# Performance work log

Measured on AMD Instinct MI355X. Metric: run time of the kernel, lower is better.

Reference implementation:

```python
import jax, jax.numpy as jnp
import numpy as np

EPS = 1e-6
NUM_HEADS = 4
GSIZE = (2, 2, 2)


def _ln_channels_first(x, w, b):
    # LayerNorm over channel dim (axis=1) of [B,C,D,H,W]
    u = x.mean(1, keepdims=True)
    s = ((x - u) ** 2).mean(1, keepdims=True)
    xn = (x - u) / jnp.sqrt(s + EPS)
    return w[None, :, None, None, None] * xn + b[None, :, None, None, None]


def setup_inputs() -> dict:
    key = jax.random.key(0)
    ks = jax.random.split(key, 7)
    B, C = 2, 256
    x2 = jax.random.normal(ks[0], (B, C, 32, 32, 32), jnp.float32)
    x1_low = jax.random.normal(ks[1], (B, C, 16, 16, 16), jnp.float32)
    sc = 1.0 / np.sqrt(C).astype(np.float32)
    q_w = jax.random.normal(ks[2], (C, C), jnp.float32) * sc
    k_w = jax.random.normal(ks[3], (C, C), jnp.float32) * sc
    v_w = jax.random.normal(ks[4], (C, C), jnp.float32) * sc
    dw_w = jax.random.normal(ks[5], (C, 1, 3, 3, 3), jnp.float32) * (1.0 / np.sqrt(27.0).astype(np.float32))
    proj_w = jax.random.normal(ks[6], (C, C), jnp.float32) * sc
    nq_w = jnp.ones((C,), jnp.float32)
    nq_b = jnp.zeros((C,), jnp.float32)
    nkv_w = jnp.ones((C,), jnp.float32)
    nkv_b = jnp.zeros((C,), jnp.float32)
    return {"x2": x2, "x1_low": x1_low, "q_w": q_w, "k_w": k_w, "v_w": v_w,
            "dw_w": dw_w, "proj_w": proj_w, "nq_w": nq_w, "nq_b": nq_b,
            "nkv_w": nkv_w, "nkv_b": nkv_b}


def reference(x2, x1_low, q_w, k_w, v_w, dw_w, proj_w, nq_w, nq_b, nkv_w, nkv_b):
    B, C, D, H, W = x2.shape
    h = NUM_HEADS
    d = C // h
    gD, gH, gW = GSIZE
    _, _, Dl, Hl, Wl = x1_low.shape

    # adaptive_avg_pool3d to (gD,gH,gW): dims divisible -> block means
    tokens = x1_low.reshape(B, C, gD, Dl // gD, gH, Hl // gH, gW, Wl // gW).mean((3, 5, 7))
    # depthwise 3x3x3 conv, padding 1
    dw = jax.lax.conv_general_dilated(
        tokens, dw_w, window_strides=(1, 1, 1), padding='SAME',
        dimension_numbers=('NCDHW', 'OIDHW', 'NCDHW'), feature_group_count=C)
    tokens = tokens + dw

    N = D * H * W
    g = gD * gH * gW

    qx = _ln_channels_first(x2, nq_w, nq_b).reshape(B, C, N)
    q = jnp.einsum('oc,bcn->bon', q_w, qx).reshape(B, h, d, N).transpose(0, 1, 3, 2)  # [B,h,N,d]

    tk = _ln_channels_first(tokens, nkv_w, nkv_b).reshape(B, C, g)
    k = jnp.einsum('oc,bcg->bog', k_w, tk).reshape(B, h, d, g)  # [B,h,d,g]
    v = jnp.einsum('oc,bcg->bog', v_w, tokens.reshape(B, C, g)).reshape(B, h, d, g).transpose(0, 1, 3, 2)  # [B,h,g,d]

    attn = jax.nn.softmax(jnp.einsum('bhnd,bhdg->bhng', q, k) / jnp.sqrt(jnp.float32(d)), axis=-1)
    out = jnp.einsum('bhng,bhgd->bhnd', attn, v)  # [B,h,N,d]
    out = out.transpose(0, 1, 3, 2).reshape(B, C, N)
    return jnp.einsum('oc,bcn->bon', proj_w, out).reshape(B, C, D, H, W)
```

## Files before the change

### kernel.cpp

```cpp
#include <hip/hip_runtime.h>
#include <math.h>

#define EPS 1e-6f

typedef __attribute__((ext_vector_type(8))) short bhalf8;
typedef __attribute__((ext_vector_type(4))) float floatx4;

__device__ __forceinline__ unsigned short f2bf(float f) {
    union { float f; unsigned u; } v; v.f = f;
    unsigned r = (v.u + 0x7fffu + ((v.u >> 16) & 1u)) >> 16;
    return (unsigned short)r;
}
__device__ __forceinline__ float bflo(unsigned u) {
    union { unsigned x; float f; } v; v.x = u << 16; return v.f;
}
__device__ __forceinline__ float bfhi(unsigned u) {
    union { unsigned x; float f; } v; v.x = u & 0xffff0000u; return v.f;
}

__global__ void pre1(const float* __restrict__ q_w,
                     const float* __restrict__ proj_w,
                     const float* __restrict__ nq_w,
                     const float* __restrict__ nq_b,
                     float* __restrict__ W1, float* __restrict__ W2,
                     unsigned short* __restrict__ W1b,
                     unsigned short* __restrict__ W2b,
                     float* __restrict__ A, float* __restrict__ Bc,
                     const float* __restrict__ x1, float* __restrict__ tokens) {
    if (blockIdx.x < 256) {
        int o = blockIdx.x;
        int c = threadIdx.x;
        float qv = q_w[o * 256 + c];
        float pv = proj_w[o * 256 + c];
        float w1 = qv * nq_w[c];
        W1[c * 256 + o] = w1;
        W2[c * 256 + o] = pv;
        int kc = c >> 5, kk = c & 31;
        W1b[kc * 8192 + o * 32 + kk] = f2bf(w1);
        W2b[kc * 8192 + o * 32 + kk] = f2bf(pv);
        float bcv = qv * nq_b[c];
        __shared__ float sA[4], sB[4];
        float a = w1, b = bcv;
        for (int off = 32; off > 0; off >>= 1) {
            a += __shfl_down(a, off);
            b += __shfl_down(b, off);
        }
        int wave = threadIdx.x >> 6, lane = threadIdx.x & 63;
        if (lane == 0) { sA[wave] = a; sB[wave] = b; }
        __syncthreads();
        if (threadIdx.x == 0) {
            A[o]  = sA[0] + sA[1] + sA[2] + sA[3];
            Bc[o] = sB[0] + sB[1] + sB[2] + sB[3];
        }
    } else {
        int bc = blockIdx.x - 256;
        const float* base = x1 + (size_t)bc * 4096;
        int wave = threadIdx.x >> 6;
        int lane = threadIdx.x & 63;
        int doff = lane >> 3, hoff = lane & 7;
        for (int t = wave * 2; t < wave * 2 + 2; ++t) {
            int gd = t >> 2, gh = (t >> 1) & 1, gw = t & 1;
            const float* p = base + (gd * 8 + doff) * 256 + (gh * 8 + hoff) * 16 + gw * 8;
            float4 v0 = *(const float4*)p;
            float4 v1 = *(const float4*)(p + 4);
            float s = v0.x + v0.y + v0.z + v0.w + v1.x + v1.y + v1.z + v1.w;
            for (int off = 32; off > 0; off >>= 1) s += __shfl_down(s, off);
            if (lane == 0) tokens[bc * 8 + t] = s * (1.0f / 512.0f);
        }
    }
}

__global__ void tokens_prep(const float* __restrict__ tokens,
                            const float* __restrict__ dw_w,
                            const float* __restrict__ nkv_w,
                            const float* __restrict__ nkv_b,
                            float* __restrict__ t2g, float* __restrict__ tng) {
    int b = blockIdx.x;
    int c = threadIdx.x;
    __shared__ float t2[256][8];
    __shared__ float u8[8], r8[8];
    float t[8];
    #pragma unroll
    for (int g = 0; g < 8; ++g) t[g] = tokens[(b * 256 + c) * 8 + g];
    float w[27];
    #pragma unroll
    for (int i = 0; i < 27; ++i) w[i] = dw_w[c * 27 + i];
    #pragma unroll
    for (int z = 0; z < 2; ++z)
    #pragma unroll
    for (int y = 0; y < 2; ++y)
    #pragma unroll
    for (int x = 0; x < 2; ++x) {
        float s = 0.f;
        #pragma unroll
        for (int i = 0; i < 3; ++i) {
            int nz = z + i - 1; if (nz < 0 || nz > 1) continue;
            #pragma unroll
            for (int j = 0; j < 3; ++j) {
                int ny = y + j - 1; if (ny < 0 || ny > 1) continue;
                #pragma unroll
                for (int l = 0; l < 3; ++l) {
                    int nx = x + l - 1; if (nx < 0 || nx > 1) continue;
                    s += w[(i * 3 + j) * 3 + l] * t[nz * 4 + ny * 2 + nx];
                }
            }
        }
        int g = z * 4 + y * 2 + x;
        t2[c][g] = t[g] + s;
    }
    __syncthreads();
    if (c < 8) {
        float su = 0.f, sq = 0.f;
        for (int cc = 0; cc < 256; ++cc) { float v = t2[cc][c]; su += v; sq += v * v; }
        float u = su * (1.f / 256.f);
        float var = sq * (1.f / 256.f) - u * u;
        u8[c] = u;
        r8[c] = rsqrtf(var + EPS);
    }
    __syncthreads();
    float nw = nkv_w[c], nb = nkv_b[c];
    #pragma unroll
    for (int g = 0; g < 8; ++g) {
        float tv = t2[c][g];
        t2g[(b * 256 + c) * 8 + g] = tv;
        tng[(b * 256 + c) * 8 + g] = nw * (tv - u8[g]) * r8[g] + nb;
    }
}

__global__ void tokens_proj(const float* __restrict__ k_w,
                            const float* __restrict__ v_w,
                            const float* __restrict__ t2g,
                            const float* __restrict__ tng,
                            float* __restrict__ kk, float* __restrict__ vv,
                            unsigned short* __restrict__ kkb) {
    int b = blockIdx.x >> 6;
    int og = blockIdx.x & 63;
    int w = threadIdx.x >> 6;
    int lane = threadIdx.x & 63;
    int o = og * 4 + w;
    float acck[8] = {0,0,0,0,0,0,0,0}, accv[8] = {0,0,0,0,0,0,0,0};
    #pragma unroll
    for (int i = 0; i < 4; ++i) {
        int c = lane + 64 * i;
        float kw = k_w[o * 256 + c];
        float vw = v_w[o * 256 + c];
        const float* tb = t2g + (size_t)(b * 256 + c) * 8;
        const float* nb = tng + (size_t)(b * 256 + c) * 8;
        float4 ta0 = *(const float4*)tb;
        float4 ta1 = *(const float4*)(tb + 4);
        float4 tn0 = *(const float4*)nb;
        float4 tn1 = *(const float4*)(nb + 4);
        acck[0] += kw * tn0.x; acck[1] += kw * tn0.y; acck[2] += kw * tn0.z; acck[3] += kw * tn0.w;
        acck[4] += kw * tn1.x; acck[5] += kw * tn1.y; acck[6] += kw * tn1.z; acck[7] += kw * tn1.w;
        accv[0] += vw * ta0.x; accv[1] += vw * ta0.y; accv[2] += vw * ta0.z; accv[3] += vw * ta0.w;
        accv[4] += vw * ta1.x; accv[5] += vw * ta1.y; accv[6] += vw * ta1.z; accv[7] += vw * ta1.w;
    }
    #pragma unroll
    for (int g = 0; g < 8; ++g)
        for (int off = 32; off > 0; off >>= 1) {
            acck[g] += __shfl_down(acck[g], off);
            accv[g] += __shfl_down(accv[g], off);
        }
    if (lane == 0) {
        #pragma unroll
        for (int g = 0; g < 8; ++g) {
            int ki = b * 2048 + o * 8 + g;
            int vi = b * 2048 + (o >> 6) * 512 + g * 64 + (o & 63);
            kk[ki] = acck[g];
            kkb[ki] = f2bf(acck[g]);
            vv[vi] = accv[g];
        }
    }
}

__global__ void ln_stats(const float* __restrict__ x2,
                         float* __restrict__ u, float* __restrict__ r) {
    int t = blockIdx.x * blockDim.x + threadIdx.x;
    int n = t << 2;
    int b = n >> 15;
    int pos = n & 32767;
    const float* p = x2 + (size_t)b * 8388608 + pos;
    float su0 = 0, su1 = 0, su2 = 0, su3 = 0;
    float sq0 = 0, sq1 = 0, sq2 = 0, sq3 = 0;
    for (int c = 0; c < 256; ++c) {
        float4 v = *(const float4*)(p + (size_t)c * 32768);
        su0 += v.x; sq0 += v.x * v.x;
        su1 += v.y; sq1 += v.y * v.y;
        su2 += v.z; sq2 += v.z * v.z;
        su3 += v.w; sq3 += v.w * v.w;
    }
    const float inv = 1.f / 256.f;
    float4 um, rm;
    um.x = su0 * inv; um.y = su1 * inv; um.z = su2 * inv; um.w = su3 * inv;
    rm.x = rsqrtf(sq0 * inv - um.x * um.x + EPS);
    rm.y = rsqrtf(sq1 * inv - um.y * um.y + EPS);
    rm.z = rsqrtf(sq2 * inv - um.z * um.z + EPS);
    rm.w = rsqrtf(sq3 * inv - um.w * um.w + EPS);
    *(float4*)(u + n) = um;
    *(float4*)(r + n) = rm;
}

__global__ __launch_bounds__(256, 3)
void fused_mfma(const float* __restrict__ x2,
                const unsigned short* __restrict__ W1b,
                const unsigned short* __restrict__ W2b,
                const float* __restrict__ Ag, const float* __restrict__ Bg,
                const unsigned short* __restrict__ kkb,
                const float* __restrict__ vvf,
                float* __restrict__ out) {
    __shared__ __align__(16) unsigned short XQ[16384];
    __shared__ __align__(16) float KVP[3072];
    __shared__ float As[256], Bs[256], us[64], rs[64];

    const int tid = threadIdx.x;
    const int w = tid >> 6;
    const int lane = tid & 63;
    const int n0g = blockIdx.x * 64;
    const int b = n0g >> 15;

    uint4  kreg  = ((const uint4*)(kkb + b * 2048))[tid];
    float4 vreg0 = ((const float4*)(vvf + b * 2048))[tid];
    float4 vreg1 = ((const float4*)(vvf + b * 2048))[256 + tid];
    As[tid] = Ag[tid];
    Bs[tid] = Bg[tid];

    {
        const int n4 = tid & 15, cg = tid >> 4;
        const float* xb = x2 + (size_t)b * 8388608 + (n0g & 32767) + n4 * 4;
        float su[4] = {0,0,0,0}, sq[4] = {0,0,0,0};
        #pragma unroll
        for (int cc = 0; cc < 8; ++cc) {
            int p = cg + 16 * cc;
            int c0 = 2 * p;
            float4 a  = *(const float4*)(xb + (size_t)c0 * 32768);
            float4 bq = *(const float4*)(xb + (size_t)(c0 + 1) * 32768);
            int g = p >> 2, wsub = p & 3;
            float av[4] = {a.x, a.y, a.z, a.w};
            float bv[4] = {bq.x, bq.y, bq.z, bq.w};
            #pragma unroll
            for (int i = 0; i < 4; ++i) {
                su[i] += av[i] + bv[i];
                sq[i] += av[i] * av[i] + bv[i] * bv[i];
                int row = 4 * n4 + i;
                int swz = ((row >> 2) ^ row) & 7;
                unsigned val = (unsigned)f2bf(av[i]) | ((unsigned)f2bf(bv[i]) << 16);
                ((unsigned*)XQ)[row * 128 + ((g ^ swz) << 2) + wsub] = val;
            }
        }
        #pragma unroll
        for (int i = 0; i < 4; ++i) {
            KVP[cg * 128 + (4 * n4 + i) * 2]     = su[i];
            KVP[cg * 128 + (4 * n4 + i) * 2 + 1] = sq[i];
        }
    }
    __syncthreads();
    if (tid < 64) {
        float S = 0, Q = 0;
        #pragma unroll
        for (int gg = 0; gg < 16; ++gg) { S += KVP[gg * 128 + tid * 2]; Q += KVP[gg * 128 + tid * 2 + 1]; }
        float mu = S * (1.f / 256.f);
        us[tid] = mu;
        rs[tid] = rsqrtf(Q * (1.f / 256.f) - mu * mu + EPS);
    }
    __syncthreads();
    unsigned short* ks = (unsigned short*)KVP;
    float* vs = KVP + 1024;
    ((uint4*)ks)[tid] = kreg;
    ((float4*)vs)[tid] = vreg0;
    ((float4*)vs)[256 + tid] = vreg1;

    const int m = lane & 15;
    const int qd = lane >> 4;

    floatx4 acc[4][4];
    #pragma unroll
    for (int i = 0; i < 4; ++i)
        #pragma unroll
        for (int j = 0; j < 4; ++j)
            acc[i][j] = (floatx4){0.f, 0.f, 0.f, 0.f};

    const unsigned short* w1p = W1b + (size_t)((4 * w) * 16 + m) * 32 + qd * 8;
    {
        bhalf8 afb[2][4];
        #pragma unroll
        for (int t = 0; t < 4; ++t) afb[0][t] = *(const bhalf8*)(w1p + t * 512);
        #pragma unroll
        for (int kc = 0; kc < 8; ++kc) {
            if (kc < 7) {
                #pragma unroll
                for (int t = 0; t < 4; ++t)
                    afb[(kc + 1) & 1][t] = *(const bhalf8*)(w1p + (kc + 1) * 8192 + t * 512);
            }
            bhalf8 bfr[4];
            #pragma unroll
            for (int nt = 0; nt < 4; ++nt) {
                int n = nt * 16 + m;
                int swz = ((n >> 2) ^ n) & 7;
                bfr[nt] = *(const bhalf8*)(XQ + n * 256 + (((4 * kc + qd) ^ swz) << 3));
            }
            #pragma unroll
            for (int t = 0; t < 4; ++t)
                #pragma unroll
                for (int nt = 0; nt < 4; ++nt)
                    acc[t][nt] = __builtin_amdgcn_mfma_f32_16x16x32_bf16(afb[kc & 1][t], bfr[nt], acc[t][nt], 0, 0, 0);
        }
    }
    __syncthreads();

    #pragma unroll
    for (int t = 0; t < 4; ++t) {
        int ob = 64 * w + 16 * t + 4 * qd;
        floatx4 Af = *(const floatx4*)&As[ob];
        floatx4 Bf = *(const floatx4*)&Bs[ob];
        int gq = ob >> 3, off = ob & 7;
        #pragma unroll
        for (int nt = 0; nt < 4; ++nt) {
            int n = nt * 16 + m;
            int swz = ((n >> 2) ^ n) & 7;
            float uv = us[n], rv = rs[n];
            unsigned p0 = (unsigned)f2bf(rv * (acc[t][nt][0] - uv * Af[0]) + Bf[0])
                        | ((unsigned)f2bf(rv * (acc[t][nt][1] - uv * Af[1]) + Bf[1]) << 16);
            unsigned p1 = (unsigned)f2bf(rv * (acc[t][nt][2] - uv * Af[2]) + Bf[2])
                        | ((unsigned)f2bf(rv * (acc[t][nt][3] - uv * Af[3]) + Bf[3]) << 16);
            uint2 val; val.x = p0; val.y = p1;
            *(uint2*)(XQ + n * 256 + ((gq ^ swz) << 3) + off) = val;
        }
    }

    {
        const int sw = ((lane >> 2) ^ lane) & 7;
        unsigned short* qrow = XQ + lane * 256;
        uint4 q4[8];
        #pragma unroll
        for (int gl = 0; gl < 8; ++gl)
            q4[gl] = *(const uint4*)(qrow + ((8 * w + (gl ^ sw)) << 3));
        float lg[8] = {0, 0, 0, 0, 0, 0, 0, 0};
        const unsigned short* kh = ks + w * 512;
        #pragma unroll
        for (int dp = 0; dp < 32; ++dp) {
            unsigned qq = ((const unsigned*)q4)[dp];
            float q0 = bflo(qq), q1 = bfhi(qq);
            uint4 k0 = *(const uint4*)(kh + dp * 16);
            uint4 k1 = *(const uint4*)(kh + dp * 16 + 8);
            lg[0] += q0 * bflo(k0.x); lg[1] += q0 * bfhi(k0.x);
            lg[2] += q0 * bflo(k0.y); lg[3] += q0 * bfhi(k0.y);
            lg[4] += q0 * bflo(k0.z); lg[5] += q0 * bfhi(k0.z);
            lg[6] += q0 * bflo(k0.w); lg[7] += q0 * bfhi(k0.w);
            lg[0] += q1 * bflo(k1.x); lg[1] += q1 * bfhi(k1.x);
            lg[2] += q1 * bflo(k1.y); lg[3] += q1 * bfhi(k1.y);
            lg[4] += q1 * bflo(k1.z); lg[5] += q1 * bfhi(k1.z);
            lg[6] += q1 * bflo(k1.w); lg[7] += q1 * bfhi(k1.w);
        }
        float mx = lg[0];
        #pragma unroll
        for (int g = 1; g < 8; ++g) mx = fmaxf(mx, lg[g]);
        float p[8], s = 0.f;
        #pragma unroll
        for (int g = 0; g < 8; ++g) { p[g] = __expf((lg[g] - mx) * 0.125f); s += p[g]; }
        float is = 1.f / s;
        #pragma unroll
        for (int g = 0; g < 8; ++g) p[g] *= is;
        float o2[64];
        #pragma unroll
        for (int j = 0; j < 64; ++j) o2[j] = 0.f;
        const float* vh = vs + w * 512;
        #pragma unroll
        for (int g = 0; g < 8; ++g) {
            float pg = p[g];
            #pragma unroll
            for (int j = 0; j < 16; ++j) {
                float4 vv4 = *(const float4*)(vh + g * 64 + j * 4);
                o2[4 * j + 0] += pg * vv4.x;
                o2[4 * j + 1] += pg * vv4.y;
                o2[4 * j + 2] += pg * vv4.z;
                o2[4 * j + 3] += pg * vv4.w;
            }
        }
        #pragma unroll
        for (int gl = 0; gl < 8; ++gl) {
            uint4 pk;
            pk.x = (unsigned)f2bf(o2[8 * gl + 0]) | ((unsigned)f2bf(o2[8 * gl + 1]) << 16);
            pk.y = (unsigned)f2bf(o2[8 * gl + 2]) | ((unsigned)f2bf(o2[8 * gl + 3]) << 16);
            pk.z = (unsigned)f2bf(o2[8 * gl + 4]) | ((unsigned)f2bf(o2[8 * gl + 5]) << 16);
            pk.w = (unsigned)f2bf(o2[8 * gl + 6]) | ((unsigned)f2bf(o2[8 * gl + 7]) << 16);
            *(uint4*)(qrow + ((8 * w + (gl ^ sw)) << 3)) = pk;
        }
    }
    __syncthreads();

    floatx4 acc2[4][4];
    #pragma unroll
    for (int i = 0; i < 4; ++i)
        #pragma unroll
        for (int j = 0; j < 4; ++j)
            acc2[i][j] = (floatx4){0.f, 0.f, 0.f, 0.f};

    const unsigned short* w2p = W2b + (size_t)((4 * w) * 16 + m) * 32 + qd * 8;
    {
        bhalf8 afb[2][4];
        #pragma unroll
        for (int t = 0; t < 4; ++t) afb[0][t] = *(const bhalf8*)(w2p + t * 512);
        #pragma unroll
        for (int kc = 0; kc < 8; ++kc) {
            if (kc < 7) {
                #pragma unroll
                for (int t = 0; t < 4; ++t)
                    afb[(kc + 1) & 1][t] = *(const bhalf8*)(w2p + (kc + 1) * 8192 + t * 512);
            }
            bhalf8 bfr[4];
            #pragma unroll
            for (int nt = 0; nt < 4; ++nt) {
                int n = nt * 16 + m;
                int swz = ((n >> 2) ^ n) & 7;
                bfr[nt] = *(const bhalf8*)(XQ + n * 256 + (((4 * kc + qd) ^ swz) << 3));
            }
            #pragma unroll
            for (int t = 0; t < 4; ++t)
                #pragma unroll
                for (int nt = 0; nt < 4; ++nt)
                    acc2[t][nt] = __builtin_amdgcn_mfma_f32_16x16x32_bf16(afb[kc & 1][t], bfr[nt], acc2[t][nt], 0, 0, 0);
        }
    }

    float* ob = out + (size_t)b * 8388608 + (n0g & 32767);
    #pragma unroll
    for (int t = 0; t < 4; ++t) {
        int o0 = 64 * w + 16 * t + 4 * qd;
        #pragma unroll
        for (int nt = 0; nt < 4; ++nt) {
            int n = nt * 16 + m;
            #pragma unroll
            for (int rr = 0; rr < 4; ++rr)
                ob[(size_t)(o0 + rr) * 32768 + n] = acc2[t][nt][rr];
        }
    }
}

#define TN 64
#define KC 16
#define QP 68

__global__ __launch_bounds__(256, 1)
void fused_main(const float* __restrict__ x2,
                const float* __restrict__ W1,
                const float* __restrict__ W2,
                const float* __restrict__ Avec,
                const float* __restrict__ Bvec,
                const float* __restrict__ uarr,
                const float* __restrict__ rarr,
                const float* __restrict__ kk,
                const float* __restrict__ vv,
                float* __restrict__ out) {
    __shared__ __align__(16) float wsm[KC * 256];
    __shared__ __align__(16) float xs[KC][72];
    __shared__ __align__(16) float qs[256][QP];
    __shared__ __align__(16) float ksm[4 * 64 * 8];
    __shared__ __align__(16) float vsm[4 * 8 * 64];

    int tid = threadIdx.x;
    int n0g = blockIdx.x * TN;
    int b = n0g >> 15;
    int pos0 = n0g & 32767;
    const float* x2b = x2 + (size_t)b * 8388608 + pos0;

    {
        const float4* kkb4 = (const float4*)(kk + b * 2048);
        const float4* vvb4 = (const float4*)(vv + b * 2048);
        for (int i = tid; i < 512; i += 256) {
            ((float4*)ksm)[i] = kkb4[i];
            ((float4*)vsm)[i] = vvb4[i];
        }
    }

    int ty = tid >> 3;
    int tx = tid & 7;
    float acc[8][8];
    #pragma unroll
    for (int i = 0; i < 8; ++i)
        #pragma unroll
        for (int j = 0; j < 8; ++j) acc[i][j] = 0.f;

    for (int kc = 0; kc < 256; kc += KC) {
        __syncthreads();
        {
            const float4* src = (const float4*)(W1 + kc * 256);
            float4* dst = (float4*)wsm;
            #pragma unroll
            for (int i = 0; i < 4; ++i) dst[tid + 256 * i] = src[tid + 256 * i];
        }
        {
            int kr = tid >> 4;
            int j4 = tid & 15;
            float4 v = *(const float4*)(x2b + (size_t)(kc + kr) * 32768 + j4 * 4);
            *(float4*)&xs[kr][j4 * 4] = v;
        }
        __syncthreads();
        #pragma unroll
        for (int k = 0; k < KC; ++k) {
            float a[8], bb[8];
            *(float4*)&a[0]  = *(float4*)&wsm[k * 256 + 8 * ty];
            *(float4*)&a[4]  = *(float4*)&wsm[k * 256 + 8 * ty + 4];
            *(float4*)&bb[0] = *(float4*)&xs[k][8 * tx];
            *(float4*)&bb[4] = *(float4*)&xs[k][8 * tx + 4];
            #pragma unroll
            for (int i = 0; i < 8; ++i)
                #pragma unroll
                for (int j = 0; j < 8; ++j)
                    acc[i][j] += a[i] * bb[j];
        }
    }

    {
        float uv[8], rv[8], Ai[8], Bi[8];
        #pragma unroll
        for (int j = 0; j < 8; ++j) { uv[j] = uarr[n0g + 8 * tx + j]; rv[j] = rarr[n0g + 8 * tx + j]; }
        #pragma unroll
        for (int i = 0; i < 8; ++i) { Ai[i] = Avec[8 * ty + i]; Bi[i] = Bvec[8 * ty + i]; }
        #pragma unroll
        for (int i = 0; i < 8; ++i)
            #pragma unroll
            for (int j = 0; j < 8; ++j)
                qs[8 * ty + i][8 * tx + j] = rv[j] * (acc[i][j] - uv[j] * Ai[i]) + Bi[i];
    }
    __syncthreads();

    {
        int n = tid & 63;
        int h = tid >> 6;
        const float* ksh = ksm + h * 512;
        const float* vsh = vsm + h * 512;
        float logit[8];
        #pragma unroll
        for (int g = 0; g < 8; ++g) logit[g] = 0.f;
        for (int d = 0; d < 64; ++d) {
            float qv = qs[h * 64 + d][n];
            #pragma unroll
            for (int g = 0; g < 8; ++g) logit[g] += qv * ksh[d * 8 + g];
        }
        float mm = logit[0];
        #pragma unroll
        for (int g = 1; g < 8; ++g) mm = fmaxf(mm, logit[g]);
        float p[8], s = 0.f;
        #pragma unroll
        for (int g = 0; g < 8; ++g) { p[g] = __expf((logit[g] - mm) * 0.125f); s += p[g]; }
        float pinv = 1.f / s;
        #pragma unroll
        for (int g = 0; g < 8; ++g) p[g] *= pinv;
        for (int d = 0; d < 64; ++d) {
            float ov = 0.f;
            #pragma unroll
            for (int g = 0; g < 8; ++g) ov += p[g] * vsh[g * 64 + d];
            qs[h * 64 + d][n] = ov;
        }
    }

    float acc2[8][8];
    #pragma unroll
    for (int i = 0; i < 8; ++i)
        #pragma unroll
        for (int j = 0; j < 8; ++j) acc2[i][j] = 0.f;

    for (int kc = 0; kc < 256; kc += KC) {
        __syncthreads();
        {
            const float4* src = (const float4*)(W2 + kc * 256);
            float4* dst = (float4*)wsm;
            #pragma unroll
            for (int i = 0; i < 4; ++i) dst[tid + 256 * i] = src[tid + 256 * i];
        }
        __syncthreads();
        #pragma unroll
        for (int k = 0; k < KC; ++k) {
            float a[8], bb[8];
            *(float4*)&a[0]  = *(float4*)&wsm[k * 256 + 8 * ty];
            *(float4*)&a[4]  = *(float4*)&wsm[k * 256 + 8 * ty + 4];
            *(float4*)&bb[0] = *(float4*)&qs[kc + k][8 * tx];
            *(float4*)&bb[4] = *(float4*)&qs[kc + k][8 * tx + 4];
            #pragma unroll
            for (int i = 0; i < 8; ++i)
                #pragma unroll
                for (int j = 0; j < 8; ++j)
                    acc2[i][j] += a[i] * bb[j];
        }
    }

    float* ob = out + (size_t)b * 8388608 + pos0;
    #pragma unroll
    for (int i = 0; i < 8; ++i) {
        float* row = ob + (size_t)(8 * ty + i) * 32768 + 8 * tx;
        *(float4*)row       = *(float4*)&acc2[i][0];
        *(float4*)(row + 4) = *(float4*)&acc2[i][4];
    }
}

extern "C" void kernel_launch(void* const* d_in, const int* in_sizes, int n_in,
                              void* d_out, int out_size, void* d_ws, size_t ws_size,
                              hipStream_t stream) {
    (void)in_sizes; (void)n_in; (void)out_size;
    const float* x2     = (const float*)d_in[0];
    const float* x1_low = (const float*)d_in[1];
    const float* q_w    = (const float*)d_in[2];
    const float* k_w    = (const float*)d_in[3];
    const float* v_w    = (const float*)d_in[4];
    const float* dw_w   = (const float*)d_in[5];
    const float* proj_w = (const float*)d_in[6];
    const float* nq_w   = (const float*)d_in[7];
    const float* nq_b   = (const float*)d_in[8];
    const float* nkv_w  = (const float*)d_in[9];
    const float* nkv_b  = (const float*)d_in[10];
    float* outp = (float*)d_out;

    float* wsf = (float*)d_ws;
    float* W1f = wsf;
    float* W2f = wsf + 65536;
    float* Av  = wsf + 131072;
    float* Bv  = wsf + 131328;
    float* u   = wsf + 131584;
    float* r   = wsf + 197120;
    float* tk  = wsf + 262656;
    float* kkf = wsf + 266752;
    float* vvf = wsf + 270848;
    unsigned short* W1b = (unsigned short*)(wsf + 274944);
    unsigned short* W2b = (unsigned short*)(wsf + 307712);
    unsigned short* kkb = (unsigned short*)(wsf + 340480);
    float* t2g = wsf + 342528;
    float* tng = wsf + 346624;
    const size_t need_bytes = (size_t)350720 * 4;

    pre1<<<768, 256, 0, stream>>>(q_w, proj_w, nq_w, nq_b, W1f, W2f, W1b, W2b, Av, Bv,
                                  x1_low, tk);
    tokens_prep<<<2, 256, 0, stream>>>(tk, dw_w, nkv_w, nkv_b, t2g, tng);
    tokens_proj<<<128, 256, 0, stream>>>(k_w, v_w, t2g, tng, kkf, vvf, kkb);

    if (ws_size >= need_bytes) {
        fused_mfma<<<1024, 256, 0, stream>>>(x2, W1b, W2b, Av, Bv, kkb, vvf, outp);
    } else {
        ln_stats<<<64, 256, 0, stream>>>(x2, u, r);
        fused_main<<<1024, 256, 0, stream>>>(x2, W1f, W2f, Av, Bv, u, r, kkf, vvf, outp);
    }
}
```

Before: 192.7 us.

## Halve fused MFMA tile to 32 tokens, fuse token kernels, stage output stores

```diff
diff --git a/kernel.cpp b/kernel.cpp
--- a/kernel.cpp
+++ b/kernel.cpp
@@ -22,7 +22,6 @@
                      const float* __restrict__ proj_w,
                      const float* __restrict__ nq_w,
                      const float* __restrict__ nq_b,
-                     float* __restrict__ W1, float* __restrict__ W2,
                      unsigned short* __restrict__ W1b,
                      unsigned short* __restrict__ W2b,
                      float* __restrict__ A, float* __restrict__ Bc,
@@ -33,8 +32,6 @@
         float qv = q_w[o * 256 + c];
         float pv = proj_w[o * 256 + c];
         float w1 = qv * nq_w[c];
-        W1[c * 256 + o] = w1;
-        W2[c * 256 + o] = pv;
         int kc = c >> 5, kk = c & 31;
         W1b[kc * 8192 + o * 32 + kk] = f2bf(w1);
         W2b[kc * 8192 + o * 32 + kk] = f2bf(pv);
@@ -70,14 +67,18 @@
     }
 }
 
-__global__ void tokens_prep(const float* __restrict__ tokens,
-                            const float* __restrict__ dw_w,
-                            const float* __restrict__ nkv_w,
-                            const float* __restrict__ nkv_b,
-                            float* __restrict__ t2g, float* __restrict__ tng) {
-    int b = blockIdx.x;
+__global__ void tokens_all(const float* __restrict__ tokens,
+                           const float* __restrict__ dw_w,
+                           const float* __restrict__ nkv_w,
+                           const float* __restrict__ nkv_b,
+                           const float* __restrict__ k_w,
+                           const float* __restrict__ v_w,
+                           unsigned short* __restrict__ kkb,
+                           float* __restrict__ vv) {
+    int b = blockIdx.x >> 6;
+    int og = blockIdx.x & 63;
     int c = threadIdx.x;
-    __shared__ float t2[256][8];
+    __shared__ float t2[256][9];
     __shared__ float u8[8], r8[8];
     float t[8];
     #pragma unroll
@@ -118,42 +119,22 @@
         r8[c] = rsqrtf(var + EPS);
     }
     __syncthreads();
-    float nw = nkv_w[c], nb = nkv_b[c];
-    #pragma unroll
-    for (int g = 0; g < 8; ++g) {
-        float tv = t2[c][g];
-        t2g[(b * 256 + c) * 8 + g] = tv;
-        tng[(b * 256 + c) * 8 + g] = nw * (tv - u8[g]) * r8[g] + nb;
-    }
-}
-
-__global__ void tokens_proj(const float* __restrict__ k_w,
-                            const float* __restrict__ v_w,
-                            const float* __restrict__ t2g,
-                            const float* __restrict__ tng,
-                            float* __restrict__ kk, float* __restrict__ vv,
-                            unsigned short* __restrict__ kkb) {
-    int b = blockIdx.x >> 6;
-    int og = blockIdx.x & 63;
-    int w = threadIdx.x >> 6;
+    int wv = threadIdx.x >> 6;
     int lane = threadIdx.x & 63;
-    int o = og * 4 + w;
+    int o = og * 4 + wv;
     float acck[8] = {0,0,0,0,0,0,0,0}, accv[8] = {0,0,0,0,0,0,0,0};
     #pragma unroll
     for (int i = 0; i < 4; ++i) {
-        int c = lane + 64 * i;
-        float kw = k_w[o * 256 + c];
-        float vw = v_w[o * 256 + c];
-        const float* tb = t2g + (size_t)(b * 256 + c) * 8;
-        const float* nb = tng + (size_t)(b * 256 + c) * 8;
-        float4 ta0 = *(const float4*)tb;
-        float4 ta1 = *(const float4*)(tb + 4);
-        float4 tn0 = *(const float4*)nb;
-        float4 tn1 = *(const float4*)(nb + 4);
-        acck[0] += kw * tn0.x; acck[1] += kw * tn0.y; acck[2] += kw * tn0.z; acck[3] += kw * tn0.w;
-        acck[4] += kw * tn1.x; acck[5] += kw * tn1.y; acck[6] += kw * tn1.z; acck[7] += kw * tn1.w;
-        accv[0] += vw * ta0.x; accv[1] += vw * ta0.y; accv[2] += vw * ta0.z; accv[3] += vw * ta0.w;
-        accv[4] += vw * ta1.x; accv[5] += vw * ta1.y; accv[6] += vw * ta1.z; accv[7] += vw * ta1.w;
+        int cc = lane + 64 * i;
+        float kw = k_w[o * 256 + cc];
+        float vw = v_w[o * 256 + cc];
+        float nw = nkv_w[cc], nb2 = nkv_b[cc];
+        #pragma unroll
+        for (int g = 0; g < 8; ++g) {
+            float tv = t2[cc][g];
+            acck[g] += kw * (nw * (tv - u8[g]) * r8[g] + nb2);
+            accv[g] += vw * tv;
+        }
     }
     #pragma unroll
     for (int g = 0; g < 8; ++g)
@@ -164,59 +145,32 @@
     if (lane == 0) {
         #pragma unroll
         for (int g = 0; g < 8; ++g) {
-            int ki = b * 2048 + o * 8 + g;
-            int vi = b * 2048 + (o >> 6) * 512 + g * 64 + (o & 63);
-            kk[ki] = acck[g];
-            kkb[ki] = f2bf(acck[g]);
-            vv[vi] = accv[g];
-        }
-    }
-}
-
-__global__ void ln_stats(const float* __restrict__ x2,
-                         float* __restrict__ u, float* __restrict__ r) {
-    int t = blockIdx.x * blockDim.x + threadIdx.x;
-    int n = t << 2;
-    int b = n >> 15;
-    int pos = n & 32767;
-    const float* p = x2 + (size_t)b * 8388608 + pos;
-    float su0 = 0, su1 = 0, su2 = 0, su3 = 0;
-    float sq0 = 0, sq1 = 0, sq2 = 0, sq3 = 0;
-    for (int c = 0; c < 256; ++c) {
-        float4 v = *(const float4*)(p + (size_t)c * 32768);
-        su0 += v.x; sq0 += v.x * v.x;
-        su1 += v.y; sq1 += v.y * v.y;
-        su2 += v.z; sq2 += v.z * v.z;
-        su3 += v.w; sq3 += v.w * v.w;
-    }
-    const float inv = 1.f / 256.f;
-    float4 um, rm;
-    um.x = su0 * inv; um.y = su1 * inv; um.z = su2 * inv; um.w = su3 * inv;
-    rm.x = rsqrtf(sq0 * inv - um.x * um.x + EPS);
-    rm.y = rsqrtf(sq1 * inv - um.y * um.y + EPS);
-    rm.z = rsqrtf(sq2 * inv - um.z * um.z + EPS);
-    rm.w = rsqrtf(sq3 * inv - um.w * um.w + EPS);
-    *(float4*)(u + n) = um;
-    *(float4*)(r + n) = rm;
-}
-
-__global__ __launch_bounds__(256, 3)
-void fused_mfma(const float* __restrict__ x2,
-                const unsigned short* __restrict__ W1b,
-                const unsigned short* __restrict__ W2b,
-                const float* __restrict__ Ag, const float* __restrict__ Bg,
-                const unsigned short* __restrict__ kkb,
-                const float* __restrict__ vvf,
-                float* __restrict__ out) {
-    __shared__ __align__(16) unsigned short XQ[16384];
+            kkb[b * 2048 + o * 8 + g] = f2bf(acck[g]);
+            vv[b * 2048 + (o >> 6) * 512 + g * 64 + (o & 63)] = accv[g];
+        }
+    }
+}
+
+__global__ __launch_bounds__(256, 5)
+void fused2(const float* __restrict__ x2,
+            const unsigned short* __restrict__ W1b,
+            const unsigned short* __restrict__ W2b,
+            const float* __restrict__ Ag, const float* __restrict__ Bg,
+            const unsigned short* __restrict__ kkb,
+            const float* __restrict__ vvf,
+            float* __restrict__ out) {
+    __shared__ __align__(16) unsigned short XQ[8192];
     __shared__ __align__(16) float KVP[3072];
-    __shared__ float As[256], Bs[256], us[64], rs[64];
+    __shared__ __align__(16) float part[256];
+    __shared__ __align__(16) float As[256], Bs[256];
+    __shared__ float us[32], rs[32];
 
     const int tid = threadIdx.x;
     const int w = tid >> 6;
     const int lane = tid & 63;
-    const int n0g = blockIdx.x * 64;
+    const int n0g = blockIdx.x * 32;
     const int b = n0g >> 15;
+    const int pos0 = n0g & 32767;
 
     uint4  kreg  = ((const uint4*)(kkb + b * 2048))[tid];
     float4 vreg0 = ((const float4*)(vvf + b * 2048))[tid];
@@ -225,12 +179,12 @@
     Bs[tid] = Bg[tid];
 
     {
-        const int n4 = tid & 15, cg = tid >> 4;
-        const float* xb = x2 + (size_t)b * 8388608 + (n0g & 32767) + n4 * 4;
+        const int n4 = tid & 7, cg = tid >> 3;
+        const float* xb = x2 + (size_t)b * 8388608 + pos0 + n4 * 4;
         float su[4] = {0,0,0,0}, sq[4] = {0,0,0,0};
         #pragma unroll
-        for (int cc = 0; cc < 8; ++cc) {
-            int p = cg + 16 * cc;
+        for (int cc = 0; cc < 4; ++cc) {
+            int p = cg + 32 * cc;
             int c0 = 2 * p;
             float4 a  = *(const float4*)(xb + (size_t)c0 * 32768);
             float4 bq = *(const float4*)(xb + (size_t)(c0 + 1) * 32768);
@@ -247,39 +201,47 @@
                 ((unsigned*)XQ)[row * 128 + ((g ^ swz) << 2) + wsub] = val;
             }
         }
+        ((uint4*)KVP)[tid] = kreg;
+        float* vs0 = KVP + 1024;
+        ((float4*)vs0)[tid]       = vreg0;
+        ((float4*)vs0)[256 + tid] = vreg1;
         #pragma unroll
         for (int i = 0; i < 4; ++i) {
-            KVP[cg * 128 + (4 * n4 + i) * 2]     = su[i];
-            KVP[cg * 128 + (4 * n4 + i) * 2 + 1] = sq[i];
+            float a2 = su[i], q2 = sq[i];
+            a2 += __shfl_down(a2, 8);  q2 += __shfl_down(q2, 8);
+            a2 += __shfl_down(a2, 16); q2 += __shfl_down(q2, 16);
+            a2 += __shfl_down(a2, 32); q2 += __shfl_down(q2, 32);
+            if (lane < 8) {
+                part[w * 64 + lane * 8 + i * 2]     = a2;
+                part[w * 64 + lane * 8 + i * 2 + 1] = q2;
+            }
         }
     }
     __syncthreads();
-    if (tid < 64) {
-        float S = 0, Q = 0;
-        #pragma unroll
-        for (int gg = 0; gg < 16; ++gg) { S += KVP[gg * 128 + tid * 2]; Q += KVP[gg * 128 + tid * 2 + 1]; }
+
+    if (tid < 32) {
+        int n4 = tid >> 2, i = tid & 3;
+        float S = 0.f, Q = 0.f;
+        #pragma unroll
+        for (int w4 = 0; w4 < 4; ++w4) {
+            S += part[w4 * 64 + n4 * 8 + i * 2];
+            Q += part[w4 * 64 + n4 * 8 + i * 2 + 1];
+        }
         float mu = S * (1.f / 256.f);
         us[tid] = mu;
         rs[tid] = rsqrtf(Q * (1.f / 256.f) - mu * mu + EPS);
     }
-    __syncthreads();
-    unsigned short* ks = (unsigned short*)KVP;
-    float* vs = KVP + 1024;
-    ((uint4*)ks)[tid] = kreg;
-    ((float4*)vs)[tid] = vreg0;
-    ((float4*)vs)[256 + tid] = vreg1;
 
     const int m = lane & 15;
     const int qd = lane >> 4;
 
-    floatx4 acc[4][4];
-    #pragma unroll
-    for (int i = 0; i < 4; ++i)
-        #pragma unroll
-        for (int j = 0; j < 4; ++j)
-            acc[i][j] = (floatx4){0.f, 0.f, 0.f, 0.f};
-
-    const unsigned short* w1p = W1b + (size_t)((4 * w) * 16 + m) * 32 + qd * 8;
+    floatx4 acc[4][2];
+    #pragma unroll
+    for (int i = 0; i < 4; ++i) {
+        acc[i][0] = (floatx4){0.f, 0.f, 0.f, 0.f};
+        acc[i][1] = (floatx4){0.f, 0.f, 0.f, 0.f};
+    }
+    const unsigned short* w1p = W1b + (size_t)(64 * w + m) * 32 + qd * 8;
     {
         bhalf8 afb[2][4];
         #pragma unroll
@@ -291,9 +253,9 @@
                 for (int t = 0; t < 4; ++t)
                     afb[(kc + 1) & 1][t] = *(const bhalf8*)(w1p + (kc + 1) * 8192 + t * 512);
             }
-            bhalf8 bfr[4];
-            #pragma unroll
-            for (int nt = 0; nt < 4; ++nt) {
+            bhalf8 bfr[2];
+            #pragma unroll
+            for (int nt = 0; nt < 2; ++nt) {
                 int n = nt * 16 + m;
                 int swz = ((n >> 2) ^ n) & 7;
                 bfr[nt] = *(const bhalf8*)(XQ + n * 256 + (((4 * kc + qd) ^ swz) << 3));
@@ -301,7 +263,7 @@
             #pragma unroll
             for (int t = 0; t < 4; ++t)
                 #pragma unroll
-                for (int nt = 0; nt < 4; ++nt)
+                for (int nt = 0; nt < 2; ++nt)
                     acc[t][nt] = __builtin_amdgcn_mfma_f32_16x16x32_bf16(afb[kc & 1][t], bfr[nt], acc[t][nt], 0, 0, 0);
         }
     }
@@ -314,7 +276,7 @@
         floatx4 Bf = *(const floatx4*)&Bs[ob];
         int gq = ob >> 3, off = ob & 7;
         #pragma unroll
-        for (int nt = 0; nt < 4; ++nt) {
+        for (int nt = 0; nt < 2; ++nt) {
             int n = nt * 16 + m;
             int swz = ((n >> 2) ^ n) & 7;
             float uv = us[n], rv = rs[n];
@@ -328,16 +290,17 @@
     }
 
     {
-        const int sw = ((lane >> 2) ^ lane) & 7;
-        unsigned short* qrow = XQ + lane * 256;
-        uint4 q4[8];
-        #pragma unroll
-        for (int gl = 0; gl < 8; ++gl)
-            q4[gl] = *(const uint4*)(qrow + ((8 * w + (gl ^ sw)) << 3));
+        const int an = lane & 31, dh = lane >> 5;
+        const int sw = ((an >> 2) ^ an) & 7;
+        unsigned short* qrow = XQ + an * 256;
+        uint4 q4[4];
+        #pragma unroll
+        for (int gl = 0; gl < 4; ++gl)
+            q4[gl] = *(const uint4*)(qrow + (((8 * w + 4 * dh + gl) ^ sw) << 3));
         float lg[8] = {0, 0, 0, 0, 0, 0, 0, 0};
-        const unsigned short* kh = ks + w * 512;
-        #pragma unroll
-        for (int dp = 0; dp < 32; ++dp) {
+        const unsigned short* kh = (const unsigned short*)KVP + w * 512 + dh * 256;
+        #pragma unroll
+        for (int dp = 0; dp < 16; ++dp) {
             unsigned qq = ((const unsigned*)q4)[dp];
             float q0 = bflo(qq), q1 = bfhi(qq);
             uint4 k0 = *(const uint4*)(kh + dp * 16);
@@ -351,6 +314,8 @@
             lg[4] += q1 * bflo(k1.z); lg[5] += q1 * bfhi(k1.z);
             lg[6] += q1 * bflo(k1.w); lg[7] += q1 * bfhi(k1.w);
         }
+        #pragma unroll
+        for (int g = 0; g < 8; ++g) lg[g] += __shfl_xor(lg[g], 32);
         float mx = lg[0];
         #pragma unroll
         for (int g = 1; g < 8; ++g) mx = fmaxf(mx, lg[g]);
@@ -360,42 +325,41 @@
         float is = 1.f / s;
         #pragma unroll
         for (int g = 0; g < 8; ++g) p[g] *= is;
-        float o2[64];
-        #pragma unroll
-        for (int j = 0; j < 64; ++j) o2[j] = 0.f;
-        const float* vh = vs + w * 512;
+        float o2[32];
+        #pragma unroll
+        for (int j = 0; j < 32; ++j) o2[j] = 0.f;
+        const float* vh = KVP + 1024 + w * 512 + dh * 32;
         #pragma unroll
         for (int g = 0; g < 8; ++g) {
             float pg = p[g];
             #pragma unroll
-            for (int j = 0; j < 16; ++j) {
-                float4 vv4 = *(const float4*)(vh + g * 64 + j * 4);
-                o2[4 * j + 0] += pg * vv4.x;
-                o2[4 * j + 1] += pg * vv4.y;
-                o2[4 * j + 2] += pg * vv4.z;
-                o2[4 * j + 3] += pg * vv4.w;
-            }
-        }
-        #pragma unroll
-        for (int gl = 0; gl < 8; ++gl) {
+            for (int j = 0; j < 8; ++j) {
+                float4 v4 = *(const float4*)(vh + g * 64 + j * 4);
+                o2[4 * j + 0] += pg * v4.x;
+                o2[4 * j + 1] += pg * v4.y;
+                o2[4 * j + 2] += pg * v4.z;
+                o2[4 * j + 3] += pg * v4.w;
+            }
+        }
+        #pragma unroll
+        for (int gl = 0; gl < 4; ++gl) {
             uint4 pk;
             pk.x = (unsigned)f2bf(o2[8 * gl + 0]) | ((unsigned)f2bf(o2[8 * gl + 1]) << 16);
             pk.y = (unsigned)f2bf(o2[8 * gl + 2]) | ((unsigned)f2bf(o2[8 * gl + 3]) << 16);
             pk.z = (unsigned)f2bf(o2[8 * gl + 4]) | ((unsigned)f2bf(o2[8 * gl + 5]) << 16);
             pk.w = (unsigned)f2bf(o2[8 * gl + 6]) | ((unsigned)f2bf(o2[8 * gl + 7]) << 16);
-            *(uint4*)(qrow + ((8 * w + (gl ^ sw)) << 3)) = pk;
+            *(uint4*)(qrow + (((8 * w + 4 * dh + gl) ^ sw) << 3)) = pk;
         }
     }
     __syncthreads();
 
-    floatx4 acc2[4][4];
-    #pragma unroll
-    for (int i = 0; i < 4; ++i)
-        #pragma unroll
-        for (int j = 0; j < 4; ++j)
-            acc2[i][j] = (floatx4){0.f, 0.f, 0.f, 0.f};
-
-    const unsigned short* w2p = W2b + (size_t)((4 * w) * 16 + m) * 32 + qd * 8;
+    floatx4 acc2[4][2];
+    #pragma unroll
+    for (int i = 0; i < 4; ++i) {
+        acc2[i][0] = (floatx4){0.f, 0.f, 0.f, 0.f};
+        acc2[i][1] = (floatx4){0.f, 0.f, 0.f, 0.f};
+    }
+    const unsigned short* w2p = W2b + (size_t)(64 * w + m) * 32 + qd * 8;
     {
         bhalf8 afb[2][4];
         #pragma unroll
@@ -407,9 +371,9 @@
                 for (int t = 0; t < 4; ++t)
                     afb[(kc + 1) & 1][t] = *(const bhalf8*)(w2p + (kc + 1) * 8192 + t * 512);
             }
-            bhalf8 bfr[4];
-            #pragma unroll
-            for (int nt = 0; nt < 4; ++nt) {
+            bhalf8 bfr[2];
+            #pragma unroll
+            for (int nt = 0; nt < 2; ++nt) {
                 int n = nt * 16 + m;
                 int swz = ((n >> 2) ^ n) & 7;
                 bfr[nt] = *(const bhalf8*)(XQ + n * 256 + (((4 * kc + qd) ^ swz) << 3));
@@ -417,186 +381,33 @@
             #pragma unroll
             for (int t = 0; t < 4; ++t)
                 #pragma unroll
-                for (int nt = 0; nt < 4; ++nt)
+                for (int nt = 0; nt < 2; ++nt)
                     acc2[t][nt] = __builtin_amdgcn_mfma_f32_16x16x32_bf16(afb[kc & 1][t], bfr[nt], acc2[t][nt], 0, 0, 0);
         }
     }
 
-    float* ob = out + (size_t)b * 8388608 + (n0g & 32767);
-    #pragma unroll
-    for (int t = 0; t < 4; ++t) {
-        int o0 = 64 * w + 16 * t + 4 * qd;
-        #pragma unroll
-        for (int nt = 0; nt < 4; ++nt) {
-            int n = nt * 16 + m;
-            #pragma unroll
-            for (int rr = 0; rr < 4; ++rr)
-                ob[(size_t)(o0 + rr) * 32768 + n] = acc2[t][nt][rr];
-        }
-    }
-}
-
-#define TN 64
-#define KC 16
-#define QP 68
-
-__global__ __launch_bounds__(256, 1)
-void fused_main(const float* __restrict__ x2,
-                const float* __restrict__ W1,
-                const float* __restrict__ W2,
-                const float* __restrict__ Avec,
-                const float* __restrict__ Bvec,
-                const float* __restrict__ uarr,
-                const float* __restrict__ rarr,
-                const float* __restrict__ kk,
-                const float* __restrict__ vv,
-                float* __restrict__ out) {
-    __shared__ __align__(16) float wsm[KC * 256];
-    __shared__ __align__(16) float xs[KC][72];
-    __shared__ __align__(16) float qs[256][QP];
-    __shared__ __align__(16) float ksm[4 * 64 * 8];
-    __shared__ __align__(16) float vsm[4 * 8 * 64];
-
-    int tid = threadIdx.x;
-    int n0g = blockIdx.x * TN;
-    int b = n0g >> 15;
-    int pos0 = n0g & 32767;
-    const float* x2b = x2 + (size_t)b * 8388608 + pos0;
-
     {
-        const float4* kkb4 = (const float4*)(kk + b * 2048);
-        const float4* vvb4 = (const float4*)(vv + b * 2048);
-        for (int i = tid; i < 512; i += 256) {
-            ((float4*)ksm)[i] = kkb4[i];
-            ((float4*)vsm)[i] = vvb4[i];
-        }
-    }
-
-    int ty = tid >> 3;
-    int tx = tid & 7;
-    float acc[8][8];
-    #pragma unroll
-    for (int i = 0; i < 8; ++i)
-        #pragma unroll
-        for (int j = 0; j < 8; ++j) acc[i][j] = 0.f;
-
-    for (int kc = 0; kc < 256; kc += KC) {
-        __syncthreads();
-        {
-            const float4* src = (const float4*)(W1 + kc * 256);
-            float4* dst = (float4*)wsm;
-            #pragma unroll
-            for (int i = 0; i < 4; ++i) dst[tid + 256 * i] = src[tid + 256 * i];
-        }
-        {
-            int kr = tid >> 4;
-            int j4 = tid & 15;
-            float4 v = *(const float4*)(x2b + (size_t)(kc + kr) * 32768 + j4 * 4);
-            *(float4*)&xs[kr][j4 * 4] = v;
-        }
-        __syncthreads();
-        #pragma unroll
-        for (int k = 0; k < KC; ++k) {
-            float a[8], bb[8];
-            *(float4*)&a[0]  = *(float4*)&wsm[k * 256 + 8 * ty];
-            *(float4*)&a[4]  = *(float4*)&wsm[k * 256 + 8 * ty + 4];
-            *(float4*)&bb[0] = *(float4*)&xs[k][8 * tx];
-            *(float4*)&bb[4] = *(float4*)&xs[k][8 * tx + 4];
-            #pragma unroll
-            for (int i = 0; i < 8; ++i)
-                #pragma unroll
-                for (int j = 0; j < 8; ++j)
-                    acc[i][j] += a[i] * bb[j];
-        }
-    }
-
-    {
-        float uv[8], rv[8], Ai[8], Bi[8];
-        #pragma unroll
-        for (int j = 0; j < 8; ++j) { uv[j] = uarr[n0g + 8 * tx + j]; rv[j] = rarr[n0g + 8 * tx + j]; }
-        #pragma unroll
-        for (int i = 0; i < 8; ++i) { Ai[i] = Avec[8 * ty + i]; Bi[i] = Bvec[8 * ty + i]; }
-        #pragma unroll
-        for (int i = 0; i < 8; ++i)
-            #pragma unroll
-            for (int j = 0; j < 8; ++j)
-                qs[8 * ty + i][8 * tx + j] = rv[j] * (acc[i][j] - uv[j] * Ai[i]) + Bi[i];
-    }
-    __syncthreads();
-
-    {
-        int n = tid & 63;
-        int h = tid >> 6;
-        const float* ksh = ksm + h * 512;
-        const float* vsh = vsm + h * 512;
-        float logit[8];
-        #pragma unroll
-        for (int g = 0; g < 8; ++g) logit[g] = 0.f;
-        for (int d = 0; d < 64; ++d) {
-            float qv = qs[h * 64 + d][n];
-            #pragma unroll
-            for (int g = 0; g < 8; ++g) logit[g] += qv * ksh[d * 8 + g];
-        }
-        float mm = logit[0];
-        #pragma unroll
-        for (int g = 1; g < 8; ++g) mm = fmaxf(mm, logit[g]);
-        float p[8], s = 0.f;
-        #pragma unroll
-        for (int g = 0; g < 8; ++g) { p[g] = __expf((logit[g] - mm) * 0.125f); s += p[g]; }
-        float pinv = 1.f / s;
-        #pragma unroll
-        for (int g = 0; g < 8; ++g) p[g] *= pinv;
-        for (int d = 0; d < 64; ++d) {
-            float ov = 0.f;
-            #pragma unroll
-            for (int g = 0; g < 8; ++g) ov += p[g] * vsh[g * 64 + d];
-            qs[h * 64 + d][n] = ov;
-        }
-    }
-
-    float acc2[8][8];
-    #pragma unroll
-    for (int i = 0; i < 8; ++i)
-        #pragma unroll
-        for (int j = 0; j < 8; ++j) acc2[i][j] = 0.f;
-
-    for (int kc = 0; kc < 256; kc += KC) {
-        __syncthreads();
-        {
-            const float4* src = (const float4*)(W2 + kc * 256);
-            float4* dst = (float4*)wsm;
-            #pragma unroll
-            for (int i = 0; i < 4; ++i) dst[tid + 256 * i] = src[tid + 256 * i];
-        }
-        __syncthreads();
-        #pragma unroll
-        for (int k = 0; k < KC; ++k) {
-            float a[8], bb[8];
-            *(float4*)&a[0]  = *(float4*)&wsm[k * 256 + 8 * ty];
-            *(float4*)&a[4]  = *(float4*)&wsm[k * 256 + 8 * ty + 4];
-            *(float4*)&bb[0] = *(float4*)&qs[kc + k][8 * tx];
-            *(float4*)&bb[4] = *(float4*)&qs[kc + k][8 * tx + 4];
-            #pragma unroll
-            for (int i = 0; i < 8; ++i)
-                #pragma unroll
-                for (int j = 0; j < 8; ++j)
-                    acc2[i][j] += a[i] * bb[j];
-        }
-    }
-
-    float* ob = out + (size_t)b * 8388608 + pos0;
-    #pragma unroll
-    for (int i = 0; i < 8; ++i) {
-        float* row = ob + (size_t)(8 * ty + i) * 32768 + 8 * tx;
-        *(float4*)row       = *(float4*)&acc2[i][0];
-        *(float4*)(row + 4) = *(float4*)&acc2[i][4];
+        float* tb = KVP + w * 320;
+        float* obase = out + (size_t)b * 8388608 + pos0;
+        const int ol = lane >> 2, c4 = lane & 3;
+        #pragma unroll
+        for (int t = 0; t < 4; ++t) {
+            #pragma unroll
+            for (int nt = 0; nt < 2; ++nt) {
+                #pragma unroll
+                for (int rr = 0; rr < 4; ++rr)
+                    tb[(qd * 4 + rr) * 20 + m] = acc2[t][nt][rr];
+                float4 vo = *(const float4*)(tb + ol * 20 + c4 * 4);
+                *(float4*)(obase + (size_t)(64 * w + 16 * t + ol) * 32768 + nt * 16 + c4 * 4) = vo;
+            }
+        }
     }
 }
 
 extern "C" void kernel_launch(void* const* d_in, const int* in_sizes, int n_in,
                               void* d_out, int out_size, void* d_ws, size_t ws_size,
                               hipStream_t stream) {
-    (void)in_sizes; (void)n_in; (void)out_size;
+    (void)in_sizes; (void)n_in; (void)out_size; (void)ws_size;
     const float* x2     = (const float*)d_in[0];
     const float* x1_low = (const float*)d_in[1];
     const float* q_w    = (const float*)d_in[2];
@@ -611,31 +422,15 @@
     float* outp = (float*)d_out;
 
     float* wsf = (float*)d_ws;
-    float* W1f = wsf;
-    float* W2f = wsf + 65536;
-    float* Av  = wsf + 131072;
-    float* Bv  = wsf + 131328;
-    float* u   = wsf + 131584;
-    float* r   = wsf + 197120;
-    float* tk  = wsf + 262656;
-    float* kkf = wsf + 266752;
-    float* vvf = wsf + 270848;
-    unsigned short* W1b = (unsigned short*)(wsf + 274944);
-    unsigned short* W2b = (unsigned short*)(wsf + 307712);
-    unsigned short* kkb = (unsigned short*)(wsf + 340480);
-    float* t2g = wsf + 342528;
-    float* tng = wsf + 346624;
-    const size_t need_bytes = (size_t)350720 * 4;
-
-    pre1<<<768, 256, 0, stream>>>(q_w, proj_w, nq_w, nq_b, W1f, W2f, W1b, W2b, Av, Bv,
-                                  x1_low, tk);
-    tokens_prep<<<2, 256, 0, stream>>>(tk, dw_w, nkv_w, nkv_b, t2g, tng);
-    tokens_proj<<<128, 256, 0, stream>>>(k_w, v_w, t2g, tng, kkf, vvf, kkb);
-
-    if (ws_size >= need_bytes) {
-        fused_mfma<<<1024, 256, 0, stream>>>(x2, W1b, W2b, Av, Bv, kkb, vvf, outp);
-    } else {
-        ln_stats<<<64, 256, 0, stream>>>(x2, u, r);
-        fused_main<<<1024, 256, 0, stream>>>(x2, W1f, W2f, Av, Bv, u, r, kkf, vvf, outp);
-    }
-}
+    float* Av  = wsf;
+    float* Bv  = wsf + 256;
+    float* tk  = wsf + 512;
+    float* vvf = wsf + 4608;
+    unsigned short* kkb = (unsigned short*)(wsf + 8704);
+    unsigned short* W1b = (unsigned short*)(wsf + 10752);
+    unsigned short* W2b = (unsigned short*)(wsf + 43520);
+
+    pre1<<<768, 256, 0, stream>>>(q_w, proj_w, nq_w, nq_b, W1b, W2b, Av, Bv, x1_low, tk);
+    tokens_all<<<128, 256, 0, stream>>>(tk, dw_w, nkv_w, nkv_b, k_w, v_w, kkb, vvf);
+    fused2<<<2048, 256, 0, stream>>>(x2, W1b, W2b, Av, Bv, kkb, vvf, outp);
+}
```

Result: faster. 187.8 us (-2.5%).
